# Optimization experiments

Measured on AMD Instinct MI355X. Metric: run time of the kernel, lower is better.

Reference implementation:

```python
import jax, jax.numpy as jnp
import numpy as np

N_OBS = 1_000_000
N_ROWS = 8192
N_COLS = 8192
RANK = 64


def setup_inputs() -> dict:
    key = jax.random.key(0)
    ks = jax.random.split(key, 7)
    vals = jax.random.normal(ks[0], (N_OBS,), dtype=jnp.float32)
    rows = jax.random.randint(ks[1], (N_OBS,), 0, N_ROWS)
    cols = jax.random.randint(ks[2], (N_OBS,), 0, N_COLS)
    stdv = 1.0 / np.sqrt(RANK)
    U = jax.random.uniform(ks[3], (N_ROWS, RANK), dtype=jnp.float32, minval=-stdv, maxval=stdv)
    V = jax.random.uniform(ks[4], (RANK, N_COLS), dtype=jnp.float32, minval=-stdv, maxval=stdv)
    sigma = jnp.ones((1,), dtype=jnp.float32)
    S_U = jax.random.normal(ks[5], (N_ROWS, N_ROWS), dtype=jnp.float32)
    S_V = jax.random.normal(ks[6], (N_COLS, N_COLS), dtype=jnp.float32)
    return {"vals": vals, "rows": rows, "cols": cols, "U": U, "V": V,
            "sigma": sigma, "S_U": S_U, "S_V": S_V}


def reference(vals, rows, cols, U, V, sigma, S_U, S_V):
    # Energy term: sum_n (t_n - U[i_n,:] . V[:,j_n])^2 / (2 sigma^2)
    u_rows = U[rows]              # [N, R] gather
    v_cols = V[:, cols].T         # [N, R] gather
    preds = jnp.einsum('nr,nr->n', u_rows, v_cols)  # [N]
    s2 = sigma[0] ** 2
    E = jnp.sum((vals - preds) ** 2) / (s2 * 2.0)
    # 0.5 * tr(U^T S_U U): per-rank quadratic forms batched into one contraction
    E = E + 0.5 * jnp.einsum('ir,ij,jr->', U, S_U, U)
    # 0.5 * tr(V S_V V^T): rows of V against S_V
    E = E + 0.5 * jnp.einsum('rn,nm,rm->', V, S_V, V)
    E = E + vals.shape[0] * jnp.log(s2)
    return E.reshape(1, 1)
```

## Files before the change

### kernel.cpp

```cpp
#include <hip/hip_runtime.h>
#include <math.h>

#define N_OBS_C  1000000
#define N_ROWS_C 8192
#define N_COLS_C 8192
#define RANK_C   64

typedef __attribute__((ext_vector_type(8))) short bf16x8;
typedef __attribute__((ext_vector_type(4))) float f32x4;

__device__ __forceinline__ unsigned short f2bf(float f) {
  union { float f; unsigned int u; } x; x.f = f;
  unsigned int u = x.u;
  unsigned int r = (u + 0x7fffu + ((u >> 16) & 1u)) >> 16;
  return (unsigned short)r;
}

__global__ void prep_kernel(const float* __restrict__ V, const float* __restrict__ U,
                            float* __restrict__ Vt, unsigned short* __restrict__ Ub,
                            unsigned short* __restrict__ Vtb) {
  int b = blockIdx.x, t = threadIdx.x;
  if (b < 128) {
    __shared__ float tile[64][65];
    int c0 = b * 64;
#pragma unroll
    for (int i = 0; i < 16; ++i) {
      int idx = i * 256 + t;
      int r = idx >> 6, c = idx & 63;
      tile[r][c] = V[r * N_COLS_C + c0 + c];
    }
    __syncthreads();
#pragma unroll
    for (int i = 0; i < 16; ++i) {
      int idx = i * 256 + t;
      int n = idx >> 6, r = idx & 63;
      float v = tile[r][n];
      Vt[(c0 + n) * RANK_C + r]  = v;
      Vtb[(c0 + n) * RANK_C + r] = f2bf(v);
    }
  } else {
    int nt  = 64 * 256;
    int tid = (b - 128) * 256 + t;
    for (int i = tid; i < N_ROWS_C * RANK_C; i += nt)
      Ub[i] = f2bf(U[i]);
  }
}

__device__ __forceinline__ void block_reduce_atomic(float v, float* out) {
#pragma unroll
  for (int off = 32; off > 0; off >>= 1) v += __shfl_down(v, off, 64);
  __shared__ float wsum[4];
  int w = threadIdx.x >> 6;
  if ((threadIdx.x & 63) == 0) wsum[w] = v;
  __syncthreads();
  if (threadIdx.x == 0) atomicAdd(out, wsum[0] + wsum[1] + wsum[2] + wsum[3]);
}

__global__ void __launch_bounds__(256)
main_kernel(const float* __restrict__ vals, const int* __restrict__ rows,
            const int* __restrict__ cols, const float* __restrict__ U,
            const float* __restrict__ sigma, const float* __restrict__ S_U,
            const float* __restrict__ S_V, const float* __restrict__ Vt,
            const unsigned short* __restrict__ Ub,
            const unsigned short* __restrict__ Vtb, float* __restrict__ out) {
  const int E_BLOCKS = 2048;
  const int TILES_PER = 64 * 64;
  int bid = blockIdx.x;
  int t = threadIdx.x;

  if (bid % 5 == 0) {
    int eb = bid / 5;
    float s2 = sigma[0] * sigma[0];
    float local = 0.f;
    int stride = E_BLOCKS * 256;
    for (int n = eb * 256 + t; n < N_OBS_C; n += stride) {
      int r = rows[n], c = cols[n];
      const f32x4* up = (const f32x4*)(U  + (size_t)r * RANK_C);
      const f32x4* vp = (const f32x4*)(Vt + (size_t)c * RANK_C);
      float d0 = 0.f, d1 = 0.f, d2 = 0.f, d3 = 0.f;
#pragma unroll
      for (int k = 0; k < 16; k += 4) {
        f32x4 a0 = up[k],     b0 = vp[k];
        f32x4 a1 = up[k + 1], b1 = vp[k + 1];
        f32x4 a2 = up[k + 2], b2 = vp[k + 2];
        f32x4 a3 = up[k + 3], b3 = vp[k + 3];
        d0 += a0[0]*b0[0] + a0[1]*b0[1] + a0[2]*b0[2] + a0[3]*b0[3];
        d1 += a1[0]*b1[0] + a1[1]*b1[1] + a1[2]*b1[2] + a1[3]*b1[3];
        d2 += a2[0]*b2[0] + a2[1]*b2[1] + a2[2]*b2[2] + a2[3]*b2[3];
        d3 += a3[0]*b3[0] + a3[1]*b3[1] + a3[2]*b3[2] + a3[3]*b3[3];
      }
      float e = vals[n] - ((d0 + d1) + (d2 + d3));
      local += e * e;
    }
    local *= 1.0f / (2.0f * s2);
    if (bid == 0 && t == 0) local += (float)N_OBS_C * logf(s2);
    block_reduce_atomic(local, out);
  } else {
    int sb = (bid / 5) * 4 + (bid % 5 - 1);
    const float* S; const unsigned short* A;
    if (sb < TILES_PER) { S = S_U; A = Ub; }
    else                { S = S_V; A = Vtb; sb -= TILES_PER; }
    int ti0 = (sb >> 6) * 128;
    int tj0 = (sb & 63) * 128;

    int w = t >> 6, lane = t & 63, quad = lane >> 4, lcol = lane & 15;

    bf16x8 af[2][2];
#pragma unroll
    for (int ti = 0; ti < 2; ++ti)
#pragma unroll
      for (int kh = 0; kh < 2; ++kh) {
        int row = ti0 + w * 32 + ti * 16 + lcol;
        af[ti][kh] = *(const bf16x8*)(A + (size_t)row * RANK_C + kh * 32 + quad * 8);
      }
    bf16x8 bf[8][2];
#pragma unroll
    for (int tj = 0; tj < 8; ++tj)
#pragma unroll
      for (int kh = 0; kh < 2; ++kh) {
        int row = tj0 + tj * 16 + lcol;
        bf[tj][kh] = *(const bf16x8*)(A + (size_t)row * RANK_C + kh * 32 + quad * 8);
      }

    f32x4 acc[2][8];
#pragma unroll
    for (int ti = 0; ti < 2; ++ti)
#pragma unroll
      for (int tj = 0; tj < 8; ++tj) {
        f32x4 z = {0.f, 0.f, 0.f, 0.f};
        z = __builtin_amdgcn_mfma_f32_16x16x32_bf16(af[ti][0], bf[tj][0], z, 0, 0, 0);
        z = __builtin_amdgcn_mfma_f32_16x16x32_bf16(af[ti][1], bf[tj][1], z, 0, 0, 0);
        acc[ti][tj] = z;
      }

    float p0 = 0.f, p1 = 0.f, p2 = 0.f, p3 = 0.f;
#pragma unroll
    for (int ti = 0; ti < 2; ++ti) {
      const float* Sb = S + (size_t)(ti0 + w * 32 + ti * 16 + quad * 4) * N_COLS_C
                          + tj0 + lcol;
#pragma unroll
      for (int tj = 0; tj < 8; ++tj) {
        p0 += Sb[0 * N_COLS_C + tj * 16] * acc[ti][tj][0];
        p1 += Sb[1 * N_COLS_C + tj * 16] * acc[ti][tj][1];
        p2 += Sb[2 * N_COLS_C + tj * 16] * acc[ti][tj][2];
        p3 += Sb[3 * N_COLS_C + tj * 16] * acc[ti][tj][3];
      }
    }
    float local = 0.5f * ((p0 + p1) + (p2 + p3));
    block_reduce_atomic(local, out);
  }
}

extern "C" void kernel_launch(void* const* d_in, const int* in_sizes, int n_in,
                              void* d_out, int out_size, void* d_ws, size_t ws_size,
                              hipStream_t stream) {
  const float* vals  = (const float*)d_in[0];
  const int*   rows  = (const int*)  d_in[1];
  const int*   cols  = (const int*)  d_in[2];
  const float* U     = (const float*)d_in[3];
  const float* V     = (const float*)d_in[4];
  const float* sigma = (const float*)d_in[5];
  const float* S_U   = (const float*)d_in[6];
  const float* S_V   = (const float*)d_in[7];
  float* out = (float*)d_out;

  char* ws = (char*)d_ws;
  float*          Vt  = (float*)ws;
  unsigned short* Ub  = (unsigned short*)(ws + 2u * 1024 * 1024);
  unsigned short* Vtb = (unsigned short*)(ws + 3u * 1024 * 1024);

  hipMemsetAsync(d_out, 0, sizeof(float), stream);
  prep_kernel<<<192, 256, 0, stream>>>(V, U, Vt, Ub, Vtb);
  main_kernel<<<10240, 256, 0, stream>>>(vals, rows, cols, U, sigma, S_U, S_V,
                                         Vt, Ub, Vtb, out);
}
```

Measured before the change: 616.2 us.

## Compute S·U via streamed MFMA over S instead of U·Uᵀ Gram tiles

```diff
diff --git a/kernel.cpp b/kernel.cpp
--- a/kernel.cpp
+++ b/kernel.cpp
@@ -2,8 +2,7 @@
 #include <math.h>
 
 #define N_OBS_C  1000000
-#define N_ROWS_C 8192
-#define N_COLS_C 8192
+#define NDIM     8192
 #define RANK_C   64
 
 typedef __attribute__((ext_vector_type(8))) short bf16x8;
@@ -16,33 +15,52 @@
   return (unsigned short)r;
 }
 
+__device__ __forceinline__ bf16x8 cvt8(f32x4 lo, f32x4 hi) {
+  bf16x8 r;
+  r[0] = (short)f2bf(lo[0]); r[1] = (short)f2bf(lo[1]);
+  r[2] = (short)f2bf(lo[2]); r[3] = (short)f2bf(lo[3]);
+  r[4] = (short)f2bf(hi[0]); r[5] = (short)f2bf(hi[1]);
+  r[6] = (short)f2bf(hi[2]); r[7] = (short)f2bf(hi[3]);
+  return r;
+}
+
 __global__ void prep_kernel(const float* __restrict__ V, const float* __restrict__ U,
-                            float* __restrict__ Vt, unsigned short* __restrict__ Ub,
-                            unsigned short* __restrict__ Vtb) {
+                            float* __restrict__ Vt, unsigned short* __restrict__ Utb,
+                            unsigned short* __restrict__ Vb) {
   int b = blockIdx.x, t = threadIdx.x;
+  __shared__ float tile[64][65];
   if (b < 128) {
-    __shared__ float tile[64][65];
     int c0 = b * 64;
 #pragma unroll
     for (int i = 0; i < 16; ++i) {
       int idx = i * 256 + t;
       int r = idx >> 6, c = idx & 63;
-      tile[r][c] = V[r * N_COLS_C + c0 + c];
+      float v = V[r * NDIM + c0 + c];
+      tile[r][c] = v;
+      Vb[r * NDIM + c0 + c] = f2bf(v);
     }
     __syncthreads();
 #pragma unroll
     for (int i = 0; i < 16; ++i) {
       int idx = i * 256 + t;
       int n = idx >> 6, r = idx & 63;
-      float v = tile[r][n];
-      Vt[(c0 + n) * RANK_C + r]  = v;
-      Vtb[(c0 + n) * RANK_C + r] = f2bf(v);
+      Vt[(c0 + n) * RANK_C + r] = tile[r][n];
     }
   } else {
-    int nt  = 64 * 256;
-    int tid = (b - 128) * 256 + t;
-    for (int i = tid; i < N_ROWS_C * RANK_C; i += nt)
-      Ub[i] = f2bf(U[i]);
+    int i0 = (b - 128) * 64;
+#pragma unroll
+    for (int i = 0; i < 16; ++i) {
+      int idx = i * 256 + t;
+      int ii = idx >> 6, r = idx & 63;
+      tile[ii][r] = U[(i0 + ii) * RANK_C + r];
+    }
+    __syncthreads();
+#pragma unroll
+    for (int i = 0; i < 16; ++i) {
+      int idx = i * 256 + t;
+      int r = idx >> 6, ii = idx & 63;
+      Utb[r * NDIM + i0 + ii] = f2bf(tile[ii][r]);
+    }
   }
 }
 
@@ -56,15 +74,14 @@
   if (threadIdx.x == 0) atomicAdd(out, wsum[0] + wsum[1] + wsum[2] + wsum[3]);
 }
 
-__global__ void __launch_bounds__(256)
+__global__ void __launch_bounds__(256, 4)
 main_kernel(const float* __restrict__ vals, const int* __restrict__ rows,
             const int* __restrict__ cols, const float* __restrict__ U,
             const float* __restrict__ sigma, const float* __restrict__ S_U,
             const float* __restrict__ S_V, const float* __restrict__ Vt,
-            const unsigned short* __restrict__ Ub,
-            const unsigned short* __restrict__ Vtb, float* __restrict__ out) {
-  const int E_BLOCKS = 2048;
-  const int TILES_PER = 64 * 64;
+            const unsigned short* __restrict__ Utb,
+            const unsigned short* __restrict__ Vb, float* __restrict__ out) {
+  const int E_BLOCKS = 256;
   int bid = blockIdx.x;
   int t = threadIdx.x;
 
@@ -97,57 +114,60 @@
     block_reduce_atomic(local, out);
   } else {
     int sb = (bid / 5) * 4 + (bid % 5 - 1);
-    const float* S; const unsigned short* A;
-    if (sb < TILES_PER) { S = S_U; A = Ub; }
-    else                { S = S_V; A = Vtb; sb -= TILES_PER; }
-    int ti0 = (sb >> 6) * 128;
-    int tj0 = (sb & 63) * 128;
+    const float* S; const unsigned short* Bt; const float* Fac;
+    if (sb < 512) { S = S_U; Bt = Utb; Fac = U; }
+    else          { S = S_V; Bt = Vb;  Fac = Vt; sb -= 512; }
+    int i0 = (sb >> 3) * 128;
+    int k0 = (sb & 7) * 1024;
 
     int w = t >> 6, lane = t & 63, quad = lane >> 4, lcol = lane & 15;
+    int row0 = i0 + w * 32;
 
-    bf16x8 af[2][2];
+    const float* Sr0 = S + (size_t)(row0 + lcol) * NDIM + k0 + quad * 8;
+    const float* Sr1 = Sr0 + (size_t)16 * NDIM;
+    const unsigned short* Bp = Bt + (size_t)lcol * NDIM + k0 + quad * 8;
+
+    f32x4 acc[2][4];
 #pragma unroll
-    for (int ti = 0; ti < 2; ++ti)
+    for (int a = 0; a < 2; ++a)
 #pragma unroll
-      for (int kh = 0; kh < 2; ++kh) {
-        int row = ti0 + w * 32 + ti * 16 + lcol;
-        af[ti][kh] = *(const bf16x8*)(A + (size_t)row * RANK_C + kh * 32 + quad * 8);
-      }
-    bf16x8 bf[8][2];
-#pragma unroll
-    for (int tj = 0; tj < 8; ++tj)
-#pragma unroll
-      for (int kh = 0; kh < 2; ++kh) {
-        int row = tj0 + tj * 16 + lcol;
-        bf[tj][kh] = *(const bf16x8*)(A + (size_t)row * RANK_C + kh * 32 + quad * 8);
-      }
+      for (int bq = 0; bq < 4; ++bq) acc[a][bq] = (f32x4){0.f, 0.f, 0.f, 0.f};
 
-    f32x4 acc[2][8];
-#pragma unroll
-    for (int ti = 0; ti < 2; ++ti)
-#pragma unroll
-      for (int tj = 0; tj < 8; ++tj) {
-        f32x4 z = {0.f, 0.f, 0.f, 0.f};
-        z = __builtin_amdgcn_mfma_f32_16x16x32_bf16(af[ti][0], bf[tj][0], z, 0, 0, 0);
-        z = __builtin_amdgcn_mfma_f32_16x16x32_bf16(af[ti][1], bf[tj][1], z, 0, 0, 0);
-        acc[ti][tj] = z;
-      }
+#pragma unroll 2
+    for (int ks = 0; ks < 32; ++ks) {
+      int koff = ks * 32;
+      f32x4 a0lo = *(const f32x4*)(Sr0 + koff);
+      f32x4 a0hi = *(const f32x4*)(Sr0 + koff + 4);
+      f32x4 a1lo = *(const f32x4*)(Sr1 + koff);
+      f32x4 a1hi = *(const f32x4*)(Sr1 + koff + 4);
+      bf16x8 b0 = *(const bf16x8*)(Bp + koff);
+      bf16x8 b1 = *(const bf16x8*)(Bp + 16 * NDIM + koff);
+      bf16x8 b2 = *(const bf16x8*)(Bp + 32 * NDIM + koff);
+      bf16x8 b3 = *(const bf16x8*)(Bp + 48 * NDIM + koff);
+      bf16x8 a0 = cvt8(a0lo, a0hi);
+      bf16x8 a1 = cvt8(a1lo, a1hi);
+      acc[0][0] = __builtin_amdgcn_mfma_f32_16x16x32_bf16(a0, b0, acc[0][0], 0, 0, 0);
+      acc[0][1] = __builtin_amdgcn_mfma_f32_16x16x32_bf16(a0, b1, acc[0][1], 0, 0, 0);
+      acc[0][2] = __builtin_amdgcn_mfma_f32_16x16x32_bf16(a0, b2, acc[0][2], 0, 0, 0);
+      acc[0][3] = __builtin_amdgcn_mfma_f32_16x16x32_bf16(a0, b3, acc[0][3], 0, 0, 0);
+      acc[1][0] = __builtin_amdgcn_mfma_f32_16x16x32_bf16(a1, b0, acc[1][0], 0, 0, 0);
+      acc[1][1] = __builtin_amdgcn_mfma_f32_16x16x32_bf16(a1, b1, acc[1][1], 0, 0, 0);
+      acc[1][2] = __builtin_amdgcn_mfma_f32_16x16x32_bf16(a1, b2, acc[1][2], 0, 0, 0);
+      acc[1][3] = __builtin_amdgcn_mfma_f32_16x16x32_bf16(a1, b3, acc[1][3], 0, 0, 0);
+    }
 
-    float p0 = 0.f, p1 = 0.f, p2 = 0.f, p3 = 0.f;
+    float p = 0.f;
 #pragma unroll
     for (int ti = 0; ti < 2; ++ti) {
-      const float* Sb = S + (size_t)(ti0 + w * 32 + ti * 16 + quad * 4) * N_COLS_C
-                          + tj0 + lcol;
+      int ib = row0 + ti * 16 + quad * 4;
 #pragma unroll
-      for (int tj = 0; tj < 8; ++tj) {
-        p0 += Sb[0 * N_COLS_C + tj * 16] * acc[ti][tj][0];
-        p1 += Sb[1 * N_COLS_C + tj * 16] * acc[ti][tj][1];
-        p2 += Sb[2 * N_COLS_C + tj * 16] * acc[ti][tj][2];
-        p3 += Sb[3 * N_COLS_C + tj * 16] * acc[ti][tj][3];
+      for (int nt = 0; nt < 4; ++nt) {
+        const float* fp = Fac + (size_t)ib * RANK_C + nt * 16 + lcol;
+        p += fp[0 * RANK_C] * acc[ti][nt][0] + fp[1 * RANK_C] * acc[ti][nt][1]
+           + fp[2 * RANK_C] * acc[ti][nt][2] + fp[3 * RANK_C] * acc[ti][nt][3];
       }
     }
-    float local = 0.5f * ((p0 + p1) + (p2 + p3));
-    block_reduce_atomic(local, out);
+    block_reduce_atomic(0.5f * p, out);
   }
 }
 
@@ -166,11 +186,11 @@
 
   char* ws = (char*)d_ws;
   float*          Vt  = (float*)ws;
-  unsigned short* Ub  = (unsigned short*)(ws + 2u * 1024 * 1024);
-  unsigned short* Vtb = (unsigned short*)(ws + 3u * 1024 * 1024);
+  unsigned short* Utb = (unsigned short*)(ws + 2u * 1024 * 1024);
+  unsigned short* Vb  = (unsigned short*)(ws + 3u * 1024 * 1024);
 
   hipMemsetAsync(d_out, 0, sizeof(float), stream);
-  prep_kernel<<<192, 256, 0, stream>>>(V, U, Vt, Ub, Vtb);
-  main_kernel<<<10240, 256, 0, stream>>>(vals, rows, cols, U, sigma, S_U, S_V,
-                                         Vt, Ub, Vtb, out);
+  prep_kernel<<<256, 256, 0, stream>>>(V, U, Vt, Utb, Vb);
+  main_kernel<<<1280, 256, 0, stream>>>(vals, rows, cols, U, sigma, S_U, S_V,
+                                        Vt, Utb, Vb, out);
 }
```

Result: slower. 741.8 us (+20.4%).

## Stage MFMA Gram tiles through LDS to vectorize S loads

Applied to the files above, without the earlier changes.

```diff
diff --git a/kernel.cpp b/kernel.cpp
--- a/kernel.cpp
+++ b/kernel.cpp
@@ -2,8 +2,7 @@
 #include <math.h>
 
 #define N_OBS_C  1000000
-#define N_ROWS_C 8192
-#define N_COLS_C 8192
+#define NDIM     8192
 #define RANK_C   64
 
 typedef __attribute__((ext_vector_type(8))) short bf16x8;
@@ -27,7 +26,7 @@
     for (int i = 0; i < 16; ++i) {
       int idx = i * 256 + t;
       int r = idx >> 6, c = idx & 63;
-      tile[r][c] = V[r * N_COLS_C + c0 + c];
+      tile[r][c] = V[r * NDIM + c0 + c];
     }
     __syncthreads();
 #pragma unroll
@@ -41,7 +40,7 @@
   } else {
     int nt  = 64 * 256;
     int tid = (b - 128) * 256 + t;
-    for (int i = tid; i < N_ROWS_C * RANK_C; i += nt)
+    for (int i = tid; i < NDIM * RANK_C; i += nt)
       Ub[i] = f2bf(U[i]);
   }
 }
@@ -56,7 +55,7 @@
   if (threadIdx.x == 0) atomicAdd(out, wsum[0] + wsum[1] + wsum[2] + wsum[3]);
 }
 
-__global__ void __launch_bounds__(256)
+__global__ void __launch_bounds__(256, 2)
 main_kernel(const float* __restrict__ vals, const int* __restrict__ rows,
             const int* __restrict__ cols, const float* __restrict__ U,
             const float* __restrict__ sigma, const float* __restrict__ S_U,
@@ -67,6 +66,8 @@
   const int TILES_PER = 64 * 64;
   int bid = blockIdx.x;
   int t = threadIdx.x;
+
+  __shared__ float gbuf[4][16][132];
 
   if (bid % 5 == 0) {
     int eb = bid / 5;
@@ -113,13 +114,13 @@
         int row = ti0 + w * 32 + ti * 16 + lcol;
         af[ti][kh] = *(const bf16x8*)(A + (size_t)row * RANK_C + kh * 32 + quad * 8);
       }
-    bf16x8 bf[8][2];
+    bf16x8 bfr[8][2];
 #pragma unroll
     for (int tj = 0; tj < 8; ++tj)
 #pragma unroll
       for (int kh = 0; kh < 2; ++kh) {
         int row = tj0 + tj * 16 + lcol;
-        bf[tj][kh] = *(const bf16x8*)(A + (size_t)row * RANK_C + kh * 32 + quad * 8);
+        bfr[tj][kh] = *(const bf16x8*)(A + (size_t)row * RANK_C + kh * 32 + quad * 8);
       }
 
     f32x4 acc[2][8];
@@ -128,26 +129,37 @@
 #pragma unroll
       for (int tj = 0; tj < 8; ++tj) {
         f32x4 z = {0.f, 0.f, 0.f, 0.f};
-        z = __builtin_amdgcn_mfma_f32_16x16x32_bf16(af[ti][0], bf[tj][0], z, 0, 0, 0);
-        z = __builtin_amdgcn_mfma_f32_16x16x32_bf16(af[ti][1], bf[tj][1], z, 0, 0, 0);
+        z = __builtin_amdgcn_mfma_f32_16x16x32_bf16(af[ti][0], bfr[tj][0], z, 0, 0, 0);
+        z = __builtin_amdgcn_mfma_f32_16x16x32_bf16(af[ti][1], bfr[tj][1], z, 0, 0, 0);
         acc[ti][tj] = z;
       }
 
-    float p0 = 0.f, p1 = 0.f, p2 = 0.f, p3 = 0.f;
+    int h = lane >> 5, l31 = lane & 31;
+    f32x4 Greg[16];
 #pragma unroll
     for (int ti = 0; ti < 2; ++ti) {
-      const float* Sb = S + (size_t)(ti0 + w * 32 + ti * 16 + quad * 4) * N_COLS_C
-                          + tj0 + lcol;
 #pragma unroll
-      for (int tj = 0; tj < 8; ++tj) {
-        p0 += Sb[0 * N_COLS_C + tj * 16] * acc[ti][tj][0];
-        p1 += Sb[1 * N_COLS_C + tj * 16] * acc[ti][tj][1];
-        p2 += Sb[2 * N_COLS_C + tj * 16] * acc[ti][tj][2];
-        p3 += Sb[3 * N_COLS_C + tj * 16] * acc[ti][tj][3];
-      }
+      for (int tj = 0; tj < 8; ++tj)
+#pragma unroll
+        for (int reg = 0; reg < 4; ++reg)
+          gbuf[w][quad * 4 + reg][tj * 16 + lcol] = acc[ti][tj][reg];
+      __syncthreads();
+#pragma unroll
+      for (int i = 0; i < 8; ++i)
+        Greg[ti * 8 + i] = *(const f32x4*)&gbuf[w][2 * i + h][4 * l31];
+      __syncthreads();
     }
-    float local = 0.5f * ((p0 + p1) + (p2 + p3));
-    block_reduce_atomic(local, out);
+
+    const float* Sp = S + (size_t)(ti0 + w * 32 + h) * NDIM + tj0 + 4 * l31;
+    f32x4 sv[16];
+#pragma unroll
+    for (int i = 0; i < 16; ++i)
+      sv[i] = *(const f32x4*)(Sp + (size_t)(2 * i) * NDIM);
+    f32x4 sum = {0.f, 0.f, 0.f, 0.f};
+#pragma unroll
+    for (int i = 0; i < 16; ++i) sum += sv[i] * Greg[i];
+    float p = (sum[0] + sum[1]) + (sum[2] + sum[3]);
+    block_reduce_atomic(0.5f * p, out);
   }
 }
 
```

Result: faster. 589.4 us (-4.4%).
